# Kernel optimization log

Measured on AMD Instinct MI355X. Metric: run time of the kernel, lower is better.

The kernel has to match this reference:

```python
import jax, jax.numpy as jnp
import numpy as np

BETA = 0.9
T = 16
THR = 1.0
SLOPE = 25.0  # snntorch surrogate.fast_sigmoid default slope


@jax.custom_vjp
def spike(x):
    # Heaviside forward, fast-sigmoid surrogate backward (snntorch fast_sigmoid)
    return (x > 0.0).astype(x.dtype)

def _spike_fwd(x):
    return spike(x), x

def _spike_bwd(x, g):
    return (g / (SLOPE * jnp.abs(x) + 1.0) ** 2,)

spike.defvjp(_spike_fwd, _spike_bwd)


def conv1d(x, w, b, pad):
    # x: (B, C_in, L), w: (C_out, C_in, K)
    y = jax.lax.conv_general_dilated(
        x, w, window_strides=(1,), padding=[(pad, pad)],
        dimension_numbers=("NCH", "OIH", "NCH"))
    return y + b[None, :, None]


def lif(cur, mem):
    # snntorch Leaky, reset_mechanism='subtract', threshold=1.0.
    # reset spike is computed from the PREVIOUS membrane and detached.
    reset = jax.lax.stop_gradient((mem > THR).astype(cur.dtype))
    mem = BETA * mem + cur - reset * THR
    spk = spike(mem - THR)
    return spk, mem


def setup_inputs() -> dict:
    key = jax.random.key(0)
    ks = jax.random.split(key, 14)

    def u(k, shape, fan_in):
        bound = 1.0 / np.sqrt(fan_in)
        return jax.random.uniform(k, shape, jnp.float32, -bound, bound)

    x = jax.random.normal(ks[0], (2048, 2, 128), dtype=jnp.float32)
    W1 = u(ks[1], (256, 2, 5), 2 * 5);    b1 = u(ks[2], (256,), 2 * 5)
    W2 = u(ks[3], (128, 256, 3), 256 * 3); b2 = u(ks[4], (128,), 256 * 3)
    W3 = u(ks[5], (64, 128, 3), 128 * 3);  b3 = u(ks[6], (64,), 128 * 3)
    W4 = u(ks[7], (2, 64, 3), 64 * 3);     b4 = u(ks[8], (2,), 64 * 3)
    fw1 = u(ks[9], (100, 256), 256);       fb1 = u(ks[10], (100,), 256)
    fw2 = u(ks[11], (40, 100), 100);       fb2 = u(ks[12], (40,), 100)
    return {"x": x, "W1": W1, "b1": b1, "W2": W2, "b2": b2,
            "W3": W3, "b3": b3, "W4": W4, "b4": b4,
            "fw1": fw1, "fb1": fb1, "fw2": fw2, "fb2": fb2}


def reference(x, W1, b1, W2, b2, W3, b3, W4, b4, fw1, fb1, fw2, fb2):
    B, _, L = x.shape
    f32 = x.dtype
    # conv1 input is constant across timesteps -> hoist (same math)
    cur1 = conv1d(x, W1, b1, 2)
    init = (jnp.zeros((B, 256, L), f32), jnp.zeros((B, 128, L), f32),
            jnp.zeros((B, 64, L), f32), jnp.zeros((B, 2, L), f32),
            jnp.zeros((B, 100), f32), jnp.zeros((B, 40), f32))

    def step(carry, _):
        m1, m2, m3, m4, m5, acc = carry
        s1, m1 = lif(cur1, m1)
        s2, m2 = lif(conv1d(s1, W2, b2, 1), m2)
        s3, m3 = lif(conv1d(s2, W3, b3, 1), m3)
        s4, m4 = lif(conv1d(s3, W4, b4, 1), m4)
        flat = s4.reshape(B, -1)                      # (B, 256)
        s5, m5 = lif(flat @ fw1.T + fb1, m5)
        acc = acc + s5 @ fw2.T + fb2
        return (m1, m2, m3, m4, m5, acc), None

    (_, _, _, _, _, acc), _ = jax.lax.scan(step, init, None, length=T)
    return acc / T
```

## Files before the change

### kernel.cpp

```cpp
#include <hip/hip_runtime.h>
#include <stdint.h>

#define BETA 0.9f

typedef unsigned short u16;
typedef unsigned char u8;
typedef signed char i8;
typedef int i32x4 __attribute__((ext_vector_type(4)));

__device__ __forceinline__ void async_copy16(const void* g, void* l) {
  __builtin_amdgcn_global_load_lds(
      (const __attribute__((address_space(1))) uint32_t*)g,
      (__attribute__((address_space(3))) uint32_t*)l, 16, 0, 0);
}

__global__ void prep_kernel(const float* __restrict__ W2, const float* __restrict__ W3,
                            const float* __restrict__ fw1, const float* __restrict__ fw2,
                            i8* __restrict__ A2c, i8* __restrict__ A3c,
                            float* __restrict__ fw1T, float* __restrict__ fw2T) {
  int o = blockIdx.x * 256 + threadIdx.x;
  if (o < 98304) {
    int tap = o >> 15, r = o & 32767, co = r >> 8, ci = r & 255;
    float w = W2[(co * 256 + ci) * 3 + tap];
    float d0 = __builtin_rintf(w * 0x1p11f);
    float r1 = w - d0 * 0x1p-11f;
    float d1 = __builtin_rintf(r1 * 0x1p18f);
    float r2 = r1 - d1 * 0x1p-18f;
    float d2 = __builtin_rintf(r2 * 0x1p25f);
    int cp = ci >> 6, cl = ci & 63;
    int ct = co >> 6, col = co & 63;
    int gs = ((cl >> 4) ^ ((col >> 1) & 3)) & 3;
    int pos = gs * 16 + (cl & 15);
    size_t base = ((size_t)((0 * 4 + cp) * 2 + ct) * 3 + tap) * 64 * 64 + col * 64 + pos;
    size_t pstride = (size_t)4 * 2 * 3 * 64 * 64;
    A2c[base] = (i8)(int)d0;
    A2c[pstride + base] = (i8)(int)d1;
    A2c[2 * pstride + base] = (i8)(int)d2;
  }
  int o2 = o - 98304;
  if (o2 >= 0 && o2 < 24576) {
    int tap = o2 >> 13, r = o2 & 8191, co = r >> 7, ci = r & 127;
    float w = W3[(co * 128 + ci) * 3 + tap];
    float d0 = __builtin_rintf(w * 0x1p11f);
    float r1 = w - d0 * 0x1p-11f;
    float d1 = __builtin_rintf(r1 * 0x1p18f);
    float r2 = r1 - d1 * 0x1p-18f;
    float d2 = __builtin_rintf(r2 * 0x1p25f);
    int cp = ci >> 6, cl = ci & 63;
    int gs = ((cl >> 4) ^ ((co >> 1) & 3)) & 3;
    int pos = gs * 16 + (cl & 15);
    size_t base = ((size_t)(0 * 2 + cp) * 3 + tap) * 64 * 64 + co * 64 + pos;
    size_t pstride = (size_t)2 * 3 * 64 * 64;
    A3c[base] = (i8)(int)d0;
    A3c[pstride + base] = (i8)(int)d1;
    A3c[2 * pstride + base] = (i8)(int)d2;
  }
  int o3 = o - (98304 + 24576);
  if (o3 >= 0 && o3 < 25600) {
    int f = o3 / 100, i = o3 % 100;
    fw1T[o3] = fw1[i * 256 + f];
  }
  int o4 = o - (98304 + 24576 + 25600);
  if (o4 >= 0 && o4 < 4000) {
    int i = o4 / 40, j = o4 % 40;
    fw2T[o4] = fw2[j * 100 + i];
  }
}

__global__ __launch_bounds__(256) void conv1_lif_kernel(
    const float* __restrict__ x, const float* __restrict__ W1,
    const float* __restrict__ b1, u8* __restrict__ SBT2) {
  __shared__ float xl[2][132];
  __shared__ u16 bl[8][128];
  int b = blockIdx.x, g = blockIdx.y;
  int tid = threadIdx.x;
  for (int i = tid; i < 264; i += 256) {
    int ci = i / 132, idx = i % 132, lg = idx - 2;
    xl[ci][idx] = (lg >= 0 && lg < 128) ? x[(b * 2 + ci) * 128 + lg] : 0.0f;
  }
  __syncthreads();
  int cosub = tid >> 5, tx = tid & 31;
  int co = g * 8 + cosub;
  float w[2][5];
#pragma unroll
  for (int ci = 0; ci < 2; ++ci)
#pragma unroll
    for (int k = 0; k < 5; ++k) w[ci][k] = W1[(co * 2 + ci) * 5 + k];
  float bias = b1[co];
  float cur[4];
#pragma unroll
  for (int j = 0; j < 4; ++j) {
    float acc = bias;
#pragma unroll
    for (int ci = 0; ci < 2; ++ci)
#pragma unroll
      for (int k = 0; k < 5; ++k) acc += w[ci][k] * xl[ci][4 * tx + j + k];
    cur[j] = acc;
  }
  float m[4] = {0.f, 0.f, 0.f, 0.f}, sp[4] = {0.f, 0.f, 0.f, 0.f};
  uint32_t bits[4] = {0u, 0u, 0u, 0u};
#pragma unroll
  for (int t = 0; t < 16; ++t) {
#pragma unroll
    for (int j = 0; j < 4; ++j) {
      m[j] = BETA * m[j] + cur[j] - sp[j];
      bool s = m[j] > 1.0f;
      bits[j] |= ((uint32_t)s) << t;
      sp[j] = s ? 1.0f : 0.0f;
    }
  }
#pragma unroll
  for (int j = 0; j < 4; ++j) bl[cosub][4 * tx + j] = (u16)bits[j];
  __syncthreads();
  if (tid < 128) {
    int l = tid;
    uint32_t wv[8];
#pragma unroll
    for (int j = 0; j < 8; ++j) wv[j] = bl[j][l];
    uint32_t ov[4];
#pragma unroll
    for (int k = 0; k < 4; ++k) {
      uint32_t v = 0;
#pragma unroll
      for (int tt = 0; tt < 4; ++tt) {
        int t = k * 4 + tt;
        uint32_t by = 0;
#pragma unroll
        for (int j = 0; j < 8; ++j) by |= ((wv[j] >> t) & 1u) << j;
        v |= by << (8 * tt);
      }
      ov[k] = v;
    }
    *(uint4*)(SBT2 + ((size_t)(b * 128 + l) * 32 + g) * 16) =
        make_uint4(ov[0], ov[1], ov[2], ov[3]);
  }
}

template <int CIN, int COUT, bool SBTOUT>
__global__ __launch_bounds__(256, 3) void conv_mfma_kernel(
    const u8* __restrict__ SBT, const i8* __restrict__ Agc,
    const float* __restrict__ bias, void* __restrict__ outp) {
  constexpr int NCP = CIN / 64;
  constexpr int NVIRT = 3 * NCP;
  constexpr int NCT = COUT / 64;
  constexpr int MT = 2;
  constexpr int NT = 8;
  constexpr int GB = CIN / 8;
  constexpr int ABYTES = 3 * 64 * 64;
  constexpr int AW = ABYTES / 4;
  constexpr int AISS = AW / 1024;
  __shared__ __align__(16) char lds[2 * ABYTES];
  __shared__ __align__(16) u8 Bs[18 * 16 * 80];

  int b = blockIdx.x, lb = blockIdx.y * 16, ct = blockIdx.z;
  int tid = threadIdx.x, lane = tid & 63, wid = tid >> 6;
  int wx = wid & 1, wy = wid >> 1;
  int q = lane >> 4, xx = lane & 15;
  int mloc = wy * 32;
  int gs16 = ((q ^ ((xx >> 1) & 3)) & 3) * 16;

  i32x4 acc[MT][NT];
#pragma unroll
  for (int mt = 0; mt < MT; ++mt)
#pragma unroll
    for (int nt = 0; nt < NT; ++nt) acc[mt][nt] = (i32x4){0, 0, 0, 0};

  auto stage_load = [&](int cp, int s) -> uint32_t {
    int row = s >> 5, gl = s & 7, tq = (s >> 3) & 3;
    int l_in = lb + row - 1;
    if ((unsigned)l_in >= 128u) return 0u;
    return *(const uint32_t*)(SBT + ((size_t)(b * 128 + l_in) * GB + cp * 8 + gl) * 16 + tq * 4);
  };
  auto stage_write = [&](int s, uint32_t w4) {
    int row = s >> 5, gl = s & 7, tq = (s >> 3) & 3;
#pragma unroll
    for (int i = 0; i < 4; ++i) {
      uint32_t by = (w4 >> (8 * i)) & 0xFFu;
      uint32_t lo = ((by & 0xFu) * 0x204081u) & 0x01010101u;
      uint32_t hi = ((by >> 4) * 0x204081u) & 0x01010101u;
      int t = tq * 4 + i;
      *(uint2*)(Bs + (row * 16 + t) * 80 + gl * 8) = make_uint2(lo, hi);
    }
  };

  uint32_t w4a = stage_load(0, tid);
  uint32_t w4b = stage_load(0, tid + 256);
  uint32_t w4c = (tid < 64) ? stage_load(0, tid + 512) : 0u;
  {
    const char* gsrc = (const char*)Agc + (size_t)ct * ABYTES +
                       (size_t)wid * AW + lane * 16;
    char* ldst = lds + wid * AW;
#pragma unroll
    for (int i = 0; i < AISS; ++i) async_copy16(gsrc + i * 1024, ldst + i * 1024);
  }

  for (int v = 0; v < NVIRT; ++v) {
    __syncthreads();
    stage_write(tid, w4a);
    stage_write(tid + 256, w4b);
    if (tid < 64) stage_write(tid + 512, w4c);
    __syncthreads();
    if (v + 1 < NVIRT) {
      const char* gsrc = (const char*)Agc + ((size_t)(v + 1) * NCT + ct) * ABYTES +
                         (size_t)wid * AW + lane * 16;
      char* ldst = lds + ((v + 1) & 1) * ABYTES + wid * AW;
#pragma unroll
      for (int i = 0; i < AISS; ++i) async_copy16(gsrc + i * 1024, ldst + i * 1024);
      int cpn = (v + 1) % NCP;
      w4a = stage_load(cpn, tid);
      w4b = stage_load(cpn, tid + 256);
      if (tid < 64) w4c = stage_load(cpn, tid + 512);
    }
    if (v > 0 && (v % NCP) == 0) {
#pragma unroll
      for (int mt = 0; mt < MT; ++mt)
#pragma unroll
        for (int nt = 0; nt < NT; ++nt) acc[mt][nt] = acc[mt][nt] << 7;
    }
    i32x4 Bf[10];
#pragma unroll
    for (int u = 0; u < 10; ++u)
      Bf[u] = *(const i32x4*)(Bs + ((wx * 8 + u) * 16 + xx) * 80 + q * 16);
    const i8* Asv = (const i8*)(lds + (v & 1) * ABYTES);
#pragma unroll
    for (int tap = 0; tap < 3; ++tap)
#pragma unroll
      for (int mt = 0; mt < MT; ++mt) {
        i32x4 Af = *(const i32x4*)(Asv + (tap * 64 + mloc + mt * 16 + xx) * 64 + gs16);
#pragma unroll
        for (int nt = 0; nt < NT; ++nt)
          acc[mt][nt] = __builtin_amdgcn_mfma_i32_16x16x64_i8(
              Af, Bf[nt + tap], acc[mt][nt], 0, 0, 0);
      }
  }
  __syncthreads();

  float* scr = (float*)(void*)lds + wid * 1216;
  u16* bl = (u16*)(lds + 19456);
#pragma unroll
  for (int mt = 0; mt < MT; ++mt) {
#pragma unroll
    for (int h = 0; h < 2; ++h) {
#pragma unroll
      for (int u2 = 0; u2 < 4; ++u2)
#pragma unroll
        for (int r = 0; r < 4; ++r)
          scr[(u2 * 16 + q * 4 + r) * 19 + xx] =
              (float)acc[mt][h * 4 + u2][r] * 0x1p-25f;
      __syncthreads();
      int col = mloc + mt * 16 + xx;
      float bc = bias[ct * 64 + col];
      const float* rowp = scr + (q * 16 + xx) * 19;
      float mm = 0.f, sp = 0.f;
      uint32_t bits = 0;
#pragma unroll
      for (int t = 0; t < 16; ++t) {
        float cur = rowp[t] + bc;
        mm = BETA * mm + cur - sp;
        bool s = mm > 1.0f;
        bits |= ((uint32_t)s) << t;
        sp = s ? 1.0f : 0.0f;
      }
      bl[col * 16 + wx * 8 + h * 4 + q] = (u16)bits;
      __syncthreads();
    }
  }

  if constexpr (SBTOUT) {
    constexpr int GBo = COUT / 8;
    if (tid < 128) {
      int g = tid & 7, ll = tid >> 3;
      uint32_t wv[8];
#pragma unroll
      for (int j = 0; j < 8; ++j) wv[j] = bl[(8 * g + j) * 16 + ll];
      uint32_t ov[4];
#pragma unroll
      for (int k = 0; k < 4; ++k) {
        uint32_t v = 0;
#pragma unroll
        for (int tt = 0; tt < 4; ++tt) {
          int t = k * 4 + tt;
          uint32_t by = 0;
#pragma unroll
          for (int j = 0; j < 8; ++j) by |= ((wv[j] >> t) & 1u) << j;
          v |= by << (8 * tt);
        }
        ov[k] = v;
      }
      *(uint4*)((u8*)outp + ((size_t)(b * 128 + lb + ll) * GBo + ct * 8 + g) * 16) =
          make_uint4(ov[0], ov[1], ov[2], ov[3]);
    }
  } else {
    if (tid < 128) {
      int col = tid >> 1, hf = tid & 1;
      uint4 v = *(const uint4*)(bl + col * 16 + hf * 8);
      *(uint4*)((u16*)outp + ((size_t)b * COUT + ct * 64 + col) * 128 + lb + hf * 8) = v;
    }
  }
}

__global__ __launch_bounds__(256) void head_kernel(
    const u16* __restrict__ s3bits, const float* __restrict__ W4,
    const float* __restrict__ b4, const float* __restrict__ fw1T,
    const float* __restrict__ fb1, const float* __restrict__ fw2T,
    const float* __restrict__ fb2, float* __restrict__ out) {
  __shared__ u16 s3l[64][130];
  __shared__ float W4l[384];
  __shared__ u16 flat4[256];
  __shared__ u16 s5b[100];
  int b = blockIdx.x, tid = threadIdx.x;

  for (int i = tid; i < 64 * 130; i += 256) {
    int ci = i / 130, idx = i % 130, lg = idx - 1;
    s3l[ci][idx] = (lg >= 0 && lg < 128) ? s3bits[((size_t)b * 64 + ci) * 128 + lg] : (u16)0;
  }
  for (int i = tid; i < 384; i += 256) W4l[i] = W4[i];
  __syncthreads();

  {
    int co = tid >> 7, l = tid & 127;
    float acc4[16];
#pragma unroll
    for (int t = 0; t < 16; ++t) acc4[t] = 0.f;
    for (int ci = 0; ci < 64; ++ci) {
#pragma unroll
      for (int k = 0; k < 3; ++k) {
        float wv = W4l[(co * 64 + ci) * 3 + k];
        uint32_t msk = s3l[ci][l + k];
#pragma unroll
        for (int t = 0; t < 16; ++t)
          acc4[t] = fmaf(wv, (float)((msk >> t) & 1u), acc4[t]);
      }
    }
    float bc = b4[co];
    float m = 0.f, sp = 0.f;
    uint32_t bits = 0;
#pragma unroll
    for (int t = 0; t < 16; ++t) {
      m = BETA * m + (acc4[t] + bc) - sp;
      bool s = m > 1.0f;
      bits |= ((uint32_t)s) << t;
      sp = s ? 1.0f : 0.0f;
    }
    flat4[tid] = (u16)bits;
  }
  __syncthreads();

  if (tid < 100) {
    float acc5[16];
#pragma unroll
    for (int t = 0; t < 16; ++t) acc5[t] = 0.f;
    for (int f = 0; f < 256; ++f) {
      float wv = fw1T[f * 100 + tid];
      uint32_t msk = flat4[f];
#pragma unroll
      for (int t = 0; t < 16; ++t)
        acc5[t] = fmaf(wv, (float)((msk >> t) & 1u), acc5[t]);
    }
    float bc = fb1[tid];
    float m = 0.f, sp = 0.f;
    uint32_t bits = 0;
#pragma unroll
    for (int t = 0; t < 16; ++t) {
      m = BETA * m + (acc5[t] + bc) - sp;
      bool s = m > 1.0f;
      bits |= ((uint32_t)s) << t;
      sp = s ? 1.0f : 0.0f;
    }
    s5b[tid] = (u16)bits;
  }
  __syncthreads();

  if (tid < 40) {
    float a = 0.f;
    for (int i = 0; i < 100; ++i) {
      float wv = fw2T[i * 40 + tid];
      a = fmaf(wv, (float)__popc((uint32_t)s5b[i]), a);
    }
    out[b * 40 + tid] = a * 0.0625f + fb2[tid];
  }
}

extern "C" void kernel_launch(void* const* d_in, const int* in_sizes, int n_in,
                              void* d_out, int out_size, void* d_ws, size_t ws_size,
                              hipStream_t stream) {
  const float* x   = (const float*)d_in[0];
  const float* W1  = (const float*)d_in[1];
  const float* b1  = (const float*)d_in[2];
  const float* W2  = (const float*)d_in[3];
  const float* b2  = (const float*)d_in[4];
  const float* W3  = (const float*)d_in[5];
  const float* b3  = (const float*)d_in[6];
  const float* W4  = (const float*)d_in[7];
  const float* b4  = (const float*)d_in[8];
  const float* fw1 = (const float*)d_in[9];
  const float* fb1 = (const float*)d_in[10];
  const float* fw2 = (const float*)d_in[11];
  const float* fb2 = (const float*)d_in[12];
  float* out = (float*)d_out;

  char* ws = (char*)d_ws;
  i8*    A2c  = (i8*)(ws);
  i8*    A3c  = (i8*)(ws + 294912);
  float* fw1T = (float*)(ws + 368640);
  float* fw2T = (float*)(ws + 471040);
  u8*    SBT2 = (u8*)(ws + 487424);
  u8*    SBT3 = (u8*)(ws + 487424 + 134217728);
  u16*   s3b  = (u16*)(ws + 487424 + 134217728 + 67108864);

  prep_kernel<<<dim3(596), dim3(256), 0, stream>>>(W2, W3, fw1, fw2, A2c, A3c, fw1T, fw2T);
  conv1_lif_kernel<<<dim3(2048, 32), dim3(256), 0, stream>>>(x, W1, b1, SBT2);
  conv_mfma_kernel<256, 128, true><<<dim3(2048, 8, 2), dim3(256), 0, stream>>>(SBT2, A2c, b2, SBT3);
  conv_mfma_kernel<128, 64, false><<<dim3(2048, 8, 1), dim3(256), 0, stream>>>(SBT3, A3c, b3, s3b);
  head_kernel<<<dim3(2048), dim3(256), 0, stream>>>(s3b, W4, b4, fw1T, fb1, fw2T, fb2, out);
}
```

Measured before the change: 1.948 ms.

## Reorder input-channel chunks to reuse staged spikes across taps, LUT-expand bits

Reorders the virtual loop over (precision plane, channel chunk) in serpentine order so consecutive iterations at plane boundaries share the same channel chunk. This lets them skip re-staging the spike tile and reloading the B fragments. It also replaces the per-byte bit-expansion arithmetic with a 256-entry LDS lookup table and precomputes the global source pointers. In the head kernel, the fc1 reduction is split across 200 threads with a partial-sum exchange through shared memory. The risks are extra LDS use for the LUT, which may lower occupancy, and a more intricate loop-index mapping.

```diff
diff --git a/kernel.cpp b/kernel.cpp
--- a/kernel.cpp
+++ b/kernel.cpp
@@ -141,16 +141,17 @@
     const u8* __restrict__ SBT, const i8* __restrict__ Agc,
     const float* __restrict__ bias, void* __restrict__ outp) {
   constexpr int NCP = CIN / 64;
+  constexpr int LNCP = (NCP == 4) ? 2 : 1;
   constexpr int NVIRT = 3 * NCP;
   constexpr int NCT = COUT / 64;
-  constexpr int MT = 2;
-  constexpr int NT = 8;
+  constexpr int MT = 2, NT = 8;
   constexpr int GB = CIN / 8;
   constexpr int ABYTES = 3 * 64 * 64;
   constexpr int AW = ABYTES / 4;
   constexpr int AISS = AW / 1024;
   __shared__ __align__(16) char lds[2 * ABYTES];
   __shared__ __align__(16) u8 Bs[18 * 16 * 80];
+  __shared__ __align__(8) uint2 LUT[256];
 
   int b = blockIdx.x, lb = blockIdx.y * 16, ct = blockIdx.z;
   int tid = threadIdx.x, lane = tid & 63, wid = tid >> 6;
@@ -159,68 +160,92 @@
   int mloc = wy * 32;
   int gs16 = ((q ^ ((xx >> 1) & 3)) & 3) * 16;
 
+  {
+    uint32_t by = tid;
+    uint32_t lo = ((by & 0xFu) * 0x204081u) & 0x01010101u;
+    uint32_t hi = (((by >> 4) & 0xFu) * 0x204081u) & 0x01010101u;
+    LUT[tid] = make_uint2(lo, hi);
+  }
+
   i32x4 acc[MT][NT];
 #pragma unroll
   for (int mt = 0; mt < MT; ++mt)
 #pragma unroll
     for (int nt = 0; nt < NT; ++nt) acc[mt][nt] = (i32x4){0, 0, 0, 0};
 
-  auto stage_load = [&](int cp, int s) -> uint32_t {
+  auto mkbase = [&](int s, const u8*& ptr, bool& vf) {
     int row = s >> 5, gl = s & 7, tq = (s >> 3) & 3;
     int l_in = lb + row - 1;
-    if ((unsigned)l_in >= 128u) return 0u;
-    return *(const uint32_t*)(SBT + ((size_t)(b * 128 + l_in) * GB + cp * 8 + gl) * 16 + tq * 4);
+    vf = ((unsigned)l_in < 128u);
+    int l_c = vf ? l_in : 0;
+    ptr = SBT + ((size_t)(b * 128 + l_c) * GB + gl) * 16 + tq * 4;
   };
+  const u8 *sp0, *sp1, *sp2 = nullptr;
+  bool f0, f1, f2 = false;
+  mkbase(tid, sp0, f0);
+  mkbase(tid + 256, sp1, f1);
+  if (tid < 64) mkbase(tid + 512, sp2, f2);
+
   auto stage_write = [&](int s, uint32_t w4) {
     int row = s >> 5, gl = s & 7, tq = (s >> 3) & 3;
-#pragma unroll
-    for (int i = 0; i < 4; ++i) {
-      uint32_t by = (w4 >> (8 * i)) & 0xFFu;
-      uint32_t lo = ((by & 0xFu) * 0x204081u) & 0x01010101u;
-      uint32_t hi = ((by >> 4) * 0x204081u) & 0x01010101u;
-      int t = tq * 4 + i;
-      *(uint2*)(Bs + (row * 16 + t) * 80 + gl * 8) = make_uint2(lo, hi);
-    }
+    u8* dst = Bs + (row * 16 + tq * 4) * 80 + gl * 8;
+#pragma unroll
+    for (int i = 0; i < 4; ++i)
+      *(uint2*)(dst + i * 80) = LUT[(w4 >> (8 * i)) & 0xFFu];
   };
 
-  uint32_t w4a = stage_load(0, tid);
-  uint32_t w4b = stage_load(0, tid + 256);
-  uint32_t w4c = (tid < 64) ? stage_load(0, tid + 512) : 0u;
+  auto ablock = [&](int v) -> size_t {
+    int p = v >> LNCP, j = v & (NCP - 1);
+    int cp = (p & 1) ? (NCP - 1 - j) : j;
+    return ((size_t)(p * NCP + cp) * NCT + ct) * (size_t)ABYTES;
+  };
+
+  uint32_t w4a = f0 ? *(const uint32_t*)sp0 : 0u;
+  uint32_t w4b = f1 ? *(const uint32_t*)sp1 : 0u;
+  uint32_t w4c = (tid < 64 && f2) ? *(const uint32_t*)sp2 : 0u;
   {
-    const char* gsrc = (const char*)Agc + (size_t)ct * ABYTES +
-                       (size_t)wid * AW + lane * 16;
+    const char* gsrc = (const char*)Agc + (size_t)wid * AW + lane * 16 + ablock(0);
     char* ldst = lds + wid * AW;
 #pragma unroll
     for (int i = 0; i < AISS; ++i) async_copy16(gsrc + i * 1024, ldst + i * 1024);
   }
 
+  i32x4 Bf[10];
   for (int v = 0; v < NVIRT; ++v) {
+    int p = v >> LNCP, j = v & (NCP - 1);
+    bool stg = (v == 0) || (j != 0);
     __syncthreads();
-    stage_write(tid, w4a);
-    stage_write(tid + 256, w4b);
-    if (tid < 64) stage_write(tid + 512, w4c);
-    __syncthreads();
+    if (stg) {
+      stage_write(tid, w4a);
+      stage_write(tid + 256, w4b);
+      if (tid < 64) stage_write(tid + 512, w4c);
+      __syncthreads();
+    }
     if (v + 1 < NVIRT) {
-      const char* gsrc = (const char*)Agc + ((size_t)(v + 1) * NCT + ct) * ABYTES +
-                         (size_t)wid * AW + lane * 16;
+      const char* gsrc = (const char*)Agc + (size_t)wid * AW + lane * 16 + ablock(v + 1);
       char* ldst = lds + ((v + 1) & 1) * ABYTES + wid * AW;
 #pragma unroll
       for (int i = 0; i < AISS; ++i) async_copy16(gsrc + i * 1024, ldst + i * 1024);
-      int cpn = (v + 1) % NCP;
-      w4a = stage_load(cpn, tid);
-      w4b = stage_load(cpn, tid + 256);
-      if (tid < 64) w4c = stage_load(cpn, tid + 512);
-    }
-    if (v > 0 && (v % NCP) == 0) {
+    }
+    if (stg) {
+      int jn = j + 1, pn = p;
+      if (jn == NCP) { pn = p + 1; jn = 1; }
+      if (pn < 3) {
+        int cpn = (pn & 1) ? (NCP - 1 - jn) : jn;
+        w4a = f0 ? *(const uint32_t*)(sp0 + cpn * 128) : 0u;
+        w4b = f1 ? *(const uint32_t*)(sp1 + cpn * 128) : 0u;
+        if (tid < 64) w4c = f2 ? *(const uint32_t*)(sp2 + cpn * 128) : 0u;
+      }
+#pragma unroll
+      for (int u = 0; u < 10; ++u)
+        Bf[u] = *(const i32x4*)(Bs + ((wx * 8 + u) * 16 + xx) * 80 + q * 16);
+    }
+    if (j == 0 && p > 0) {
 #pragma unroll
       for (int mt = 0; mt < MT; ++mt)
 #pragma unroll
         for (int nt = 0; nt < NT; ++nt) acc[mt][nt] = acc[mt][nt] << 7;
     }
-    i32x4 Bf[10];
-#pragma unroll
-    for (int u = 0; u < 10; ++u)
-      Bf[u] = *(const i32x4*)(Bs + ((wx * 8 + u) * 16 + xx) * 80 + q * 16);
     const i8* Asv = (const i8*)(lds + (v & 1) * ABYTES);
 #pragma unroll
     for (int tap = 0; tap < 3; ++tap)
@@ -272,7 +297,7 @@
       int g = tid & 7, ll = tid >> 3;
       uint32_t wv[8];
 #pragma unroll
-      for (int j = 0; j < 8; ++j) wv[j] = bl[(8 * g + j) * 16 + ll];
+      for (int j2 = 0; j2 < 8; ++j2) wv[j2] = bl[(8 * g + j2) * 16 + ll];
       uint32_t ov[4];
 #pragma unroll
       for (int k = 0; k < 4; ++k) {
@@ -282,7 +307,7 @@
           int t = k * 4 + tt;
           uint32_t by = 0;
 #pragma unroll
-          for (int j = 0; j < 8; ++j) by |= ((wv[j] >> t) & 1u) << j;
+          for (int j2 = 0; j2 < 8; ++j2) by |= ((wv[j2] >> t) & 1u) << j2;
           v |= by << (8 * tt);
         }
         ov[k] = v;
@@ -346,23 +371,34 @@
   }
   __syncthreads();
 
-  if (tid < 100) {
-    float acc5[16];
-#pragma unroll
-    for (int t = 0; t < 16; ++t) acc5[t] = 0.f;
-    for (int f = 0; f < 256; ++f) {
-      float wv = fw1T[f * 100 + tid];
-      uint32_t msk = flat4[f];
+  float* part5 = (float*)&s3l[0][0];
+  float acc5[16];
+#pragma unroll
+  for (int t = 0; t < 16; ++t) acc5[t] = 0.f;
+  int n5 = tid % 100, h5 = tid / 100;
+  if (tid < 200) {
+    const float* wp = fw1T + (h5 * 128) * 100 + n5;
+    for (int f = 0; f < 128; ++f) {
+      float wv = wp[f * 100];
+      uint32_t msk = flat4[h5 * 128 + f];
 #pragma unroll
       for (int t = 0; t < 16; ++t)
         acc5[t] = fmaf(wv, (float)((msk >> t) & 1u), acc5[t]);
     }
+    if (h5 == 1) {
+#pragma unroll
+      for (int t = 0; t < 16; ++t) part5[n5 * 16 + t] = acc5[t];
+    }
+  }
+  __syncthreads();
+  if (tid < 100) {
     float bc = fb1[tid];
     float m = 0.f, sp = 0.f;
     uint32_t bits = 0;
 #pragma unroll
     for (int t = 0; t < 16; ++t) {
-      m = BETA * m + (acc5[t] + bc) - sp;
+      float cur = acc5[t] + part5[tid * 16 + t] + bc;
+      m = BETA * m + cur - sp;
       bool s = m > 1.0f;
       bits |= ((uint32_t)s) << t;
       sp = s ? 1.0f : 0.0f;
```

After: 1.850 ms. 5.0% less time.
